# Kernel optimization log

Hardware: AMD Instinct MI355X
Metric: run time of the kernel (lower is better)

## Reference

```python
import jax, jax.numpy as jnp
import numpy as np

NUM_CLASSES = 1000
B, Q, N = 64, 900, 30
NO_OBJ_W = 0.1
COST_CLASS, COST_BBOX, COST_GIOU = 1.0, 5.0, 2.0
LOSS_BBOX, LOSS_GIOU = 5.0, 2.0


def cxcywh_to_xyxy(b):
    cx, cy, w, h = b[..., 0], b[..., 1], b[..., 2], b[..., 3]
    return jnp.stack([cx - 0.5 * w, cy - 0.5 * h, cx + 0.5 * w, cy + 0.5 * h], axis=-1)


def _area(b):
    return jnp.clip(b[..., 2] - b[..., 0], 0.0) * jnp.clip(b[..., 3] - b[..., 1], 0.0)


def giou_xyxy(b1, b2):
    # GIoU over broadcastable [..., 4] xyxy boxes
    lt = jnp.maximum(b1[..., :2], b2[..., :2])
    rb = jnp.minimum(b1[..., 2:], b2[..., 2:])
    wh = jnp.clip(rb - lt, 0.0)
    inter = wh[..., 0] * wh[..., 1]
    union = _area(b1) + _area(b2) - inter
    iou = inter / jnp.maximum(union, 1e-6)
    ltc = jnp.minimum(b1[..., :2], b2[..., :2])
    rbc = jnp.maximum(b1[..., 2:], b2[..., 2:])
    whc = jnp.clip(rbc - ltc, 0.0)
    ac = whc[..., 0] * whc[..., 1]
    return iou - (ac - union) / jnp.maximum(ac, 1e-6)


def _cost_matrices(pred_logits, pred_boxes, tgt_labels, tgt_boxes_xyxy):
    prob = jax.nn.softmax(pred_logits, axis=-1)                    # [B,Q,C+1]
    cost_cls = -jax.vmap(lambda p, l: p[:, l])(prob, tgt_labels)   # [B,Q,N]
    pred_xyxy = jnp.clip(cxcywh_to_xyxy(pred_boxes), 0.0, 1.0)     # [B,Q,4]
    cost_l1 = jnp.sum(jnp.abs(pred_xyxy[:, :, None] - tgt_boxes_xyxy[:, None]), -1)
    cost_g = -giou_xyxy(pred_xyxy[:, :, None], tgt_boxes_xyxy[:, None])
    C = COST_CLASS * cost_cls + COST_BBOX * cost_l1 + COST_GIOU * cost_g
    return C, pred_xyxy


def greedy_match(C):
    # faithful to the module's torch fallback matcher: iteratively pick the
    # global minimum of the cost matrix, masking used rows/cols (host-side,
    # non-differentiable, exactly like the detach->cpu->assignment in torch)
    Cw = C.copy()
    Qn, Nn = Cw.shape
    rows, cols = [], []
    for _ in range(min(Qn, Nn)):
        i = int(np.argmin(Cw))
        pi, ti = divmod(i, Nn)
        rows.append(pi)
        cols.append(ti)
        Cw[pi, :] = 1e9
        Cw[:, ti] = 1e9
    return np.array(rows, dtype=np.int32), np.array(cols, dtype=np.int32)


def match_all(Cnp):
    pis, tis = zip(*[greedy_match(Cnp[b]) for b in range(Cnp.shape[0])])
    return jnp.asarray(np.stack(pis)), jnp.asarray(np.stack(tis))  # [B,N] each


def set_losses(pred_logits, pred_xyxy, tgt_labels, tgt_boxes_xyxy, pi, ti):
    ce_weight = jnp.ones(NUM_CLASSES + 1, jnp.float32).at[NUM_CLASSES].set(NO_OBJ_W)
    bidx = jnp.arange(B)[:, None]
    # target class per query: matched -> tgt label, else no-object class
    tc = jnp.full((B, Q), NUM_CLASSES, dtype=jnp.int32)
    tc = tc.at[bidx, pi].set(jnp.take_along_axis(tgt_labels, ti, axis=1))
    nll = -jnp.take_along_axis(jax.nn.log_softmax(pred_logits, -1), tc[..., None].astype(jnp.int32), axis=2)[..., 0]
    w = ce_weight[tc]
    ce = jnp.mean(jnp.sum(w * nll, axis=1) / jnp.sum(w, axis=1))  # torch weighted CE mean, per image
    p_m = pred_xyxy[bidx, pi]          # [B,N,4] matched preds
    t_m = tgt_boxes_xyxy[bidx, ti]     # [B,N,4] matched targets
    l1 = jnp.mean(jnp.mean(jnp.abs(p_m - t_m), axis=(1, 2)))
    gl = jnp.mean(jnp.mean(1.0 - giou_xyxy(p_m, t_m), axis=1))
    total = ce + LOSS_BBOX * l1 + LOSS_GIOU * gl
    return jnp.stack([total, ce, l1, gl])


def setup_inputs():
    key = jax.random.key(0)
    k1, k2, k3, k4, k5 = jax.random.split(key, 5)
    pred_logits = jax.random.normal(k1, (B, Q, NUM_CLASSES + 1), jnp.float32)
    pred_boxes = jax.random.uniform(k2, (B, Q, 4), jnp.float32, 0.05, 0.95)
    tgt_labels = jax.random.randint(k3, (B, N), 0, NUM_CLASSES, dtype=jnp.int32)
    lt = jax.random.uniform(k4, (B, N, 2), jnp.float32, 0.0, 0.6)
    wh = jax.random.uniform(k5, (B, N, 2), jnp.float32, 0.02, 0.37)
    tgt_boxes_xyxy = jnp.concatenate([lt, lt + wh], axis=-1)  # valid 0..1 xyxy
    return {"pred_logits": pred_logits, "pred_boxes": pred_boxes,
            "tgt_labels": tgt_labels, "tgt_boxes_xyxy": tgt_boxes_xyxy}


def reference(pred_logits, pred_boxes, tgt_labels, tgt_boxes_xyxy):
    C, pred_xyxy = _cost_matrices(pred_logits, pred_boxes, tgt_labels, tgt_boxes_xyxy)
    pi, ti = match_all(np.asarray(jax.lax.stop_gradient(C)))
    # returns [loss_total, loss_ce, loss_bbox, loss_giou]
    return set_losses(pred_logits, pred_xyxy, tgt_labels, tgt_boxes_xyxy, pi, ti)
```

## Files before the change

kernel.cpp:

```cpp
#include <hip/hip_runtime.h>
#include <math.h>

#define BB 64
#define QQ 900
#define NN 30
#define C1 1001
#define QN (QQ * NN)
#define NO_OBJ_W 0.1f

__device__ unsigned g_ord[BB * QN];
__device__ unsigned long long g_top[BB * NN * NN];
__device__ float  g_logZ[BB * QQ];
__device__ float  g_noobj[BB * QQ];
__device__ float4 g_xyxy[BB * QQ];
__device__ float  g_acc[3];
__device__ unsigned g_cnt;

__device__ __forceinline__ float giou_f(float ax1, float ay1, float ax2, float ay2,
                                        float bx1, float by1, float bx2, float by2) {
    float ix1 = fmaxf(ax1, bx1), iy1 = fmaxf(ay1, by1);
    float ix2 = fminf(ax2, bx2), iy2 = fminf(ay2, by2);
    float iw = fmaxf(ix2 - ix1, 0.f), ih = fmaxf(iy2 - iy1, 0.f);
    float inter = iw * ih;
    float areaA = fmaxf(ax2 - ax1, 0.f) * fmaxf(ay2 - ay1, 0.f);
    float areaB = fmaxf(bx2 - bx1, 0.f) * fmaxf(by2 - by1, 0.f);
    float uni = areaA + areaB - inter;
    float iou = inter / fmaxf(uni, 1e-6f);
    float cx1 = fminf(ax1, bx1), cy1 = fminf(ay1, by1);
    float cx2 = fmaxf(ax2, bx2), cy2 = fmaxf(ay2, by2);
    float cw = fmaxf(cx2 - cx1, 0.f), ch = fmaxf(cy2 - cy1, 0.f);
    float ac = cw * ch;
    return iou - (ac - uni) / fmaxf(ac, 1e-6f);
}

__device__ __forceinline__ unsigned ord_map(float f) {
    unsigned u = __float_as_uint(f);
    return (u & 0x80000000u) ? ~u : (u | 0x80000000u);
}

__global__ __launch_bounds__(256) void cost_kernel(const float* __restrict__ logits,
                                                   const float* __restrict__ pboxes,
                                                   const int*   __restrict__ labels,
                                                   const float* __restrict__ tboxes) {
    if (blockIdx.x == 0 && threadIdx.x == 0) {
        g_acc[0] = 0.f; g_acc[1] = 0.f; g_acc[2] = 0.f;
        g_cnt = 0u;
    }
    int gwave = (blockIdx.x * blockDim.x + threadIdx.x) >> 6;
    int lane = threadIdx.x & 63;
    if (gwave >= BB * QQ) return;
    int b = gwave / QQ;

    size_t s = (size_t)gwave * C1;
    size_t a0 = (s + 3) >> 2;
    size_t a1 = (s + C1) >> 2;
    int nq = (int)(a1 - a0);
    int hh = (int)(a0 * 4 - s);
    int tt = (int)((s + C1) - a1 * 4);
    const float4* L4 = (const float4*)logits;

    float4 v4[4];
#pragma unroll
    for (int i = 0; i < 4; ++i) {
        int qq = lane + 64 * i;
        v4[i] = (qq < nq) ? L4[a0 + qq]
                          : make_float4(-INFINITY, -INFINITY, -INFINITY, -INFINITY);
    }
    float e1 = (lane < hh) ? logits[s + lane] : -INFINITY;
    float e2 = (lane < tt) ? logits[a1 * 4 + lane] : -INFINITY;

    float mx = fmaxf(e1, e2);
#pragma unroll
    for (int i = 0; i < 4; ++i)
        mx = fmaxf(mx, fmaxf(fmaxf(v4[i].x, v4[i].y), fmaxf(v4[i].z, v4[i].w)));
#pragma unroll
    for (int off = 32; off; off >>= 1) mx = fmaxf(mx, __shfl_xor(mx, off));

    float sm = __expf(e1 - mx) + __expf(e2 - mx);
#pragma unroll
    for (int i = 0; i < 4; ++i) {
        sm += __expf(v4[i].x - mx);
        sm += __expf(v4[i].y - mx);
        sm += __expf(v4[i].z - mx);
        sm += __expf(v4[i].w - mx);
    }
#pragma unroll
    for (int off = 32; off; off >>= 1) sm += __shfl_xor(sm, off);
    float logZ = mx + __logf(sm);

    float row1000 = logits[s + 1000];

    const float* pb = pboxes + (size_t)gwave * 4;
    float cx = pb[0], cy = pb[1], w = pb[2], h = pb[3];
    float x1 = fminf(fmaxf(cx - 0.5f * w, 0.f), 1.f);
    float y1 = fminf(fmaxf(cy - 0.5f * h, 0.f), 1.f);
    float x2 = fminf(fmaxf(cx + 0.5f * w, 0.f), 1.f);
    float y2 = fminf(fmaxf(cy + 0.5f * h, 0.f), 1.f);

    if (lane == 0) {
        g_logZ[gwave] = logZ;
        g_noobj[gwave] = logZ - row1000;
        g_xyxy[gwave] = make_float4(x1, y1, x2, y2);
    }

    if (lane < NN) {
        int t = lane;
        int lab = labels[b * NN + t];
        float pcls = __expf(logits[s + lab] - logZ);
        const float* tb = tboxes + ((size_t)(b * NN + t)) * 4;
        float tx1 = tb[0], ty1 = tb[1], tx2 = tb[2], ty2 = tb[3];
        float l1 = fabsf(x1 - tx1) + fabsf(y1 - ty1) + fabsf(x2 - tx2) + fabsf(y2 - ty2);
        float g = giou_f(x1, y1, x2, y2, tx1, ty1, tx2, ty2);
        g_ord[(size_t)gwave * NN + t] = ord_map(-pcls + 5.0f * l1 - 2.0f * g);
    }
}

__global__ __launch_bounds__(256) void select_kernel() {
    int gw = (blockIdx.x * blockDim.x + threadIdx.x) >> 6;
    int lane = threadIdx.x & 63;
    if (gw >= BB * NN) return;
    int b = gw / NN;
    int t = gw - b * NN;

    unsigned long long key[16];
    if (lane < 60) {
#pragma unroll
        for (int j = 0; j < 15; ++j) {
            int q = j * 60 + lane;
            unsigned o = g_ord[((size_t)(b * QQ + q)) * NN + t];
            key[j] = ((unsigned long long)o << 32) | (unsigned)(q * NN + t);
        }
    } else {
#pragma unroll
        for (int j = 0; j < 15; ++j) key[j] = ~0ull;
    }
    key[15] = ~0ull;

#pragma unroll
    for (int kk = 2; kk <= 16; kk <<= 1) {
#pragma unroll
        for (int jj = kk >> 1; jj > 0; jj >>= 1) {
#pragma unroll
            for (int i = 0; i < 16; ++i) {
                int l = i ^ jj;
                if (l > i) {
                    bool up = ((i & kk) == 0);
                    unsigned long long a = key[i], c = key[l];
                    bool sw = up ? (a > c) : (a < c);
                    key[i] = sw ? c : a;
                    key[l] = sw ? a : c;
                }
            }
        }
    }

    unsigned long long* outp = g_top + (size_t)gw * NN;
#pragma unroll 1
    for (int r = 0; r < NN / 2; ++r) {
        unsigned long long m1 = key[0];
        unsigned long long m2 = key[1];
#pragma unroll
        for (int off = 32; off; off >>= 1) {
            unsigned long long o1 = __shfl_xor(m1, off);
            unsigned long long o2 = __shfl_xor(m2, off);
            unsigned long long lo = (o1 < m1) ? o1 : m1;
            unsigned long long hi = (o1 < m1) ? m1 : o1;
            unsigned long long n2 = (o2 < m2) ? o2 : m2;
            m1 = lo;
            m2 = (hi < n2) ? hi : n2;
        }
        if (lane == 2 * r)     outp[2 * r]     = m1;
        if (lane == 2 * r + 1) outp[2 * r + 1] = m2;
        if (key[0] == m1 || key[0] == m2) {
#pragma unroll
            for (int j = 0; j < 15; ++j) key[j] = key[j + 1];
            key[15] = ~0ull;
        }
        if (key[0] == m2) {
#pragma unroll
            for (int j = 0; j < 15; ++j) key[j] = key[j + 1];
            key[15] = ~0ull;
        }
    }
}

__global__ __launch_bounds__(256) void match_loss_kernel(const float* __restrict__ logits,
                                                         const int*   __restrict__ labels,
                                                         const float* __restrict__ tboxes,
                                                         float* __restrict__ out) {
    int b = blockIdx.x;
    int tid = threadIdx.x;

    __shared__ unsigned long long s_cand[NN * NN];
    __shared__ int s_pi[NN], s_ti[NN];
    __shared__ unsigned s_dead[29];
    __shared__ float s4[4][4];

    const unsigned long long* topb = g_top + (size_t)b * NN * NN;
    for (int i = tid; i < NN * NN; i += 256) s_cand[i] = topb[i];
    if (tid < 29) s_dead[tid] = 0u;
    __syncthreads();

    if (tid < 64) {
        int lane = tid;
        bool colLive = lane < NN;
        int ptr = 0;
        unsigned long long cand = colLive ? s_cand[lane * NN] : ~0ull;
        unsigned rowc = colLive ? ((unsigned)cand) / NN : 0u;

        int it = 0;
        while (it < NN) {
            unsigned long long m1 = colLive ? cand : ~0ull;
            unsigned long long m2 = ~0ull;
#pragma unroll
            for (int off = 32; off; off >>= 1) {
                unsigned long long o1 = __shfl_xor(m1, off);
                unsigned long long o2 = __shfl_xor(m2, off);
                unsigned long long lo = (o1 < m1) ? o1 : m1;
                unsigned long long hi = (o1 < m1) ? m1 : o1;
                unsigned long long n2 = (o2 < m2) ? o2 : m2;
                m1 = lo;
                m2 = (hi < n2) ? hi : n2;
            }
            unsigned e1 = (unsigned)m1;
            int q1 = e1 / NN, t1 = e1 - (e1 / NN) * NN;
            unsigned e2 = (unsigned)m2;
            int q2 = e2 / NN, t2 = e2 - (e2 / NN) * NN;
            bool acc2 = (m2 != ~0ull) && (it + 1 < NN) && (q2 != q1) && (t2 != t1);

            if (lane == 0) {
                s_pi[it] = q1;
                s_ti[it] = t1;
                s_dead[q1 >> 5] |= (1u << (q1 & 31));
                if (acc2) {
                    s_pi[it + 1] = q2;
                    s_ti[it + 1] = t2;
                    s_dead[q2 >> 5] |= (1u << (q2 & 31));
                }
            }
            if (lane == t1) colLive = false;
            if (acc2 && lane == t2) colLive = false;
            if (colLive && (rowc == (unsigned)q1 || (acc2 && rowc == (unsigned)q2))) {
                do {
                    ++ptr;
                    cand = s_cand[lane * NN + ptr];
                    rowc = ((unsigned)cand) / NN;
                } while ((s_dead[rowc >> 5] >> (rowc & 31)) & 1u);
            }
            it += acc2 ? 2 : 1;
        }
    }
    __syncthreads();

    float sA = 0.f;
    for (int q = tid; q < QQ; q += 256) sA += g_noobj[b * QQ + q];

    float sB = 0.f, sL = 0.f, sG = 0.f;
    if (tid < NN) {
        int pq = s_pi[tid], pt = s_ti[tid];
        int gq = b * QQ + pq;
        int lab = labels[b * NN + pt];
        float mnll = g_logZ[gq] - logits[(size_t)gq * C1 + lab];
        sB = mnll - NO_OBJ_W * g_noobj[gq];
        float4 p = g_xyxy[gq];
        const float* tb = tboxes + ((size_t)(b * NN + pt)) * 4;
        float tx1 = tb[0], ty1 = tb[1], tx2 = tb[2], ty2 = tb[3];
        sL = fabsf(p.x - tx1) + fabsf(p.y - ty1) + fabsf(p.z - tx2) + fabsf(p.w - ty2);
        sG = 1.0f - giou_f(p.x, p.y, p.z, p.w, tx1, ty1, tx2, ty2);
    }

    int lane = tid & 63, wid = tid >> 6;
    float vv[4] = {sA, sB, sL, sG};
#pragma unroll
    for (int j = 0; j < 4; ++j) {
        float x = vv[j];
#pragma unroll
        for (int off = 32; off; off >>= 1) x += __shfl_xor(x, off);
        if (lane == 0) s4[wid][j] = x;
    }
    __syncthreads();
    if (tid == 0) {
        float a = 0.f, bs = 0.f, l = 0.f, g = 0.f;
        for (int w = 0; w < 4; ++w) { a += s4[w][0]; bs += s4[w][1]; l += s4[w][2]; g += s4[w][3]; }
        atomicAdd(&g_acc[0], NO_OBJ_W * a + bs);
        atomicAdd(&g_acc[1], l);
        atomicAdd(&g_acc[2], g);
        __threadfence();
        unsigned prev = atomicAdd(&g_cnt, 1u);
        if (prev == BB - 1) {
            __threadfence();
            float ce = atomicAdd(&g_acc[0], 0.f) / (float)(BB * 117);
            float l1 = atomicAdd(&g_acc[1], 0.f) / (float)(BB * NN * 4);
            float gl = atomicAdd(&g_acc[2], 0.f) / (float)(BB * NN);
            out[0] = ce + 5.0f * l1 + 2.0f * gl;
            out[1] = ce;
            out[2] = l1;
            out[3] = gl;
        }
    }
}

extern "C" void kernel_launch(void* const* d_in, const int* in_sizes, int n_in,
                              void* d_out, int out_size, void* d_ws, size_t ws_size,
                              hipStream_t stream) {
    const float* pred_logits = (const float*)d_in[0];
    const float* pred_boxes  = (const float*)d_in[1];
    const int*   tgt_labels  = (const int*)d_in[2];
    const float* tgt_boxes   = (const float*)d_in[3];
    float* out = (float*)d_out;

    cost_kernel<<<(BB * QQ) / 4, 256, 0, stream>>>(pred_logits, pred_boxes, tgt_labels, tgt_boxes);
    select_kernel<<<(BB * NN) / 4, 256, 0, stream>>>();
    match_loss_kernel<<<BB, 256, 0, stream>>>(pred_logits, tgt_labels, tgt_boxes, out);
}
```

Measured before the change: 94.44 us.

## Fuse top-k selection into matching kernel with LDS-staged cost ordering

```diff
diff --git a/kernel.cpp b/kernel.cpp
--- a/kernel.cpp
+++ b/kernel.cpp
@@ -7,9 +7,10 @@
 #define C1 1001
 #define QN (QQ * NN)
 #define NO_OBJ_W 0.1f
+#define MTB 512
+#define LDW 31
 
 __device__ unsigned g_ord[BB * QN];
-__device__ unsigned long long g_top[BB * NN * NN];
 __device__ float  g_logZ[BB * QQ];
 __device__ float  g_noobj[BB * QQ];
 __device__ float4 g_xyxy[BB * QQ];
@@ -115,94 +116,100 @@
     }
 }
 
-__global__ __launch_bounds__(256) void select_kernel() {
-    int gw = (blockIdx.x * blockDim.x + threadIdx.x) >> 6;
-    int lane = threadIdx.x & 63;
-    if (gw >= BB * NN) return;
-    int b = gw / NN;
-    int t = gw - b * NN;
-
-    unsigned long long key[16];
-    if (lane < 60) {
-#pragma unroll
-        for (int j = 0; j < 15; ++j) {
-            int q = j * 60 + lane;
-            unsigned o = g_ord[((size_t)(b * QQ + q)) * NN + t];
-            key[j] = ((unsigned long long)o << 32) | (unsigned)(q * NN + t);
-        }
-    } else {
-#pragma unroll
-        for (int j = 0; j < 15; ++j) key[j] = ~0ull;
-    }
-    key[15] = ~0ull;
-
-#pragma unroll
-    for (int kk = 2; kk <= 16; kk <<= 1) {
-#pragma unroll
-        for (int jj = kk >> 1; jj > 0; jj >>= 1) {
-#pragma unroll
-            for (int i = 0; i < 16; ++i) {
-                int l = i ^ jj;
-                if (l > i) {
-                    bool up = ((i & kk) == 0);
-                    unsigned long long a = key[i], c = key[l];
-                    bool sw = up ? (a > c) : (a < c);
-                    key[i] = sw ? c : a;
-                    key[l] = sw ? a : c;
-                }
-            }
-        }
-    }
-
-    unsigned long long* outp = g_top + (size_t)gw * NN;
-#pragma unroll 1
-    for (int r = 0; r < NN / 2; ++r) {
-        unsigned long long m1 = key[0];
-        unsigned long long m2 = key[1];
-#pragma unroll
-        for (int off = 32; off; off >>= 1) {
-            unsigned long long o1 = __shfl_xor(m1, off);
-            unsigned long long o2 = __shfl_xor(m2, off);
-            unsigned long long lo = (o1 < m1) ? o1 : m1;
-            unsigned long long hi = (o1 < m1) ? m1 : o1;
-            unsigned long long n2 = (o2 < m2) ? o2 : m2;
-            m1 = lo;
-            m2 = (hi < n2) ? hi : n2;
-        }
-        if (lane == 2 * r)     outp[2 * r]     = m1;
-        if (lane == 2 * r + 1) outp[2 * r + 1] = m2;
-        if (key[0] == m1 || key[0] == m2) {
-#pragma unroll
-            for (int j = 0; j < 15; ++j) key[j] = key[j + 1];
-            key[15] = ~0ull;
-        }
-        if (key[0] == m2) {
-#pragma unroll
-            for (int j = 0; j < 15; ++j) key[j] = key[j + 1];
-            key[15] = ~0ull;
-        }
-    }
-}
-
-__global__ __launch_bounds__(256) void match_loss_kernel(const float* __restrict__ logits,
-                                                         const int*   __restrict__ labels,
-                                                         const float* __restrict__ tboxes,
-                                                         float* __restrict__ out) {
+__global__ __launch_bounds__(MTB, 1) void sml_kernel(const float* __restrict__ logits,
+                                                     const int*   __restrict__ labels,
+                                                     const float* __restrict__ tboxes,
+                                                     float* __restrict__ out) {
     int b = blockIdx.x;
     int tid = threadIdx.x;
-
+    int lane = tid & 63, wid = tid >> 6;
+
+    __shared__ unsigned s_ord[QQ * LDW];
     __shared__ unsigned long long s_cand[NN * NN];
     __shared__ int s_pi[NN], s_ti[NN];
     __shared__ unsigned s_dead[29];
-    __shared__ float s4[4][4];
-
-    const unsigned long long* topb = g_top + (size_t)b * NN * NN;
-    for (int i = tid; i < NN * NN; i += 256) s_cand[i] = topb[i];
+    __shared__ float s4[MTB / 64][4];
+
+    const uint4* src4 = (const uint4*)(g_ord + (size_t)b * QN);
+    for (int i = tid; i < QN / 4; i += MTB) {
+        uint4 v = src4[i];
+        int f = 4 * i;
+        int q = f / NN, t = f - q * NN;
+        unsigned vals[4] = {v.x, v.y, v.z, v.w};
+#pragma unroll
+        for (int k = 0; k < 4; ++k) {
+            int fk = f + k;
+            int qk = fk / NN, tk = fk - qk * NN;
+            s_ord[qk * LDW + tk] = vals[k];
+        }
+    }
+    __syncthreads();
+
+    for (int c = wid; c < NN; c += MTB / 64) {
+        unsigned long long key[16];
+        if (lane < 60) {
+#pragma unroll
+            for (int j = 0; j < 15; ++j) {
+                int q = j * 60 + lane;
+                unsigned o = s_ord[q * LDW + c];
+                key[j] = ((unsigned long long)o << 32) | (unsigned)(q * NN + c);
+            }
+        } else {
+#pragma unroll
+            for (int j = 0; j < 15; ++j) key[j] = ~0ull;
+        }
+        key[15] = ~0ull;
+
+#pragma unroll
+        for (int kk = 2; kk <= 16; kk <<= 1) {
+#pragma unroll
+            for (int jj = kk >> 1; jj > 0; jj >>= 1) {
+#pragma unroll
+                for (int i = 0; i < 16; ++i) {
+                    int l = i ^ jj;
+                    if (l > i) {
+                        bool up = ((i & kk) == 0);
+                        unsigned long long a = key[i], cc = key[l];
+                        bool sw = up ? (a > cc) : (a < cc);
+                        key[i] = sw ? cc : a;
+                        key[l] = sw ? a : cc;
+                    }
+                }
+            }
+        }
+
+#pragma unroll 1
+        for (int r = 0; r < NN / 2; ++r) {
+            unsigned long long m1 = key[0];
+            unsigned long long m2 = key[1];
+#pragma unroll
+            for (int off = 32; off; off >>= 1) {
+                unsigned long long o1 = __shfl_xor(m1, off);
+                unsigned long long o2 = __shfl_xor(m2, off);
+                unsigned long long lo = (o1 < m1) ? o1 : m1;
+                unsigned long long hi = (o1 < m1) ? m1 : o1;
+                unsigned long long n2 = (o2 < m2) ? o2 : m2;
+                m1 = lo;
+                m2 = (hi < n2) ? hi : n2;
+            }
+            if (lane == 2 * r)     s_cand[c * NN + 2 * r]     = m1;
+            if (lane == 2 * r + 1) s_cand[c * NN + 2 * r + 1] = m2;
+            if (key[0] == m1 || key[0] == m2) {
+#pragma unroll
+                for (int j = 0; j < 15; ++j) key[j] = key[j + 1];
+                key[15] = ~0ull;
+            }
+            if (key[0] == m2) {
+#pragma unroll
+                for (int j = 0; j < 15; ++j) key[j] = key[j + 1];
+                key[15] = ~0ull;
+            }
+        }
+    }
     if (tid < 29) s_dead[tid] = 0u;
     __syncthreads();
 
     if (tid < 64) {
-        int lane = tid;
         bool colLive = lane < NN;
         int ptr = 0;
         unsigned long long cand = colLive ? s_cand[lane * NN] : ~0ull;
@@ -253,7 +260,7 @@
     __syncthreads();
 
     float sA = 0.f;
-    for (int q = tid; q < QQ; q += 256) sA += g_noobj[b * QQ + q];
+    for (int q = tid; q < QQ; q += MTB) sA += g_noobj[b * QQ + q];
 
     float sB = 0.f, sL = 0.f, sG = 0.f;
     if (tid < NN) {
@@ -269,7 +276,6 @@
         sG = 1.0f - giou_f(p.x, p.y, p.z, p.w, tx1, ty1, tx2, ty2);
     }
 
-    int lane = tid & 63, wid = tid >> 6;
     float vv[4] = {sA, sB, sL, sG};
 #pragma unroll
     for (int j = 0; j < 4; ++j) {
@@ -281,7 +287,9 @@
     __syncthreads();
     if (tid == 0) {
         float a = 0.f, bs = 0.f, l = 0.f, g = 0.f;
-        for (int w = 0; w < 4; ++w) { a += s4[w][0]; bs += s4[w][1]; l += s4[w][2]; g += s4[w][3]; }
+        for (int w = 0; w < MTB / 64; ++w) {
+            a += s4[w][0]; bs += s4[w][1]; l += s4[w][2]; g += s4[w][3];
+        }
         atomicAdd(&g_acc[0], NO_OBJ_W * a + bs);
         atomicAdd(&g_acc[1], l);
         atomicAdd(&g_acc[2], g);
@@ -310,6 +318,5 @@
     float* out = (float*)d_out;
 
     cost_kernel<<<(BB * QQ) / 4, 256, 0, stream>>>(pred_logits, pred_boxes, tgt_labels, tgt_boxes);
-    select_kernel<<<(BB * NN) / 4, 256, 0, stream>>>();
-    match_loss_kernel<<<BB, 256, 0, stream>>>(pred_logits, tgt_labels, tgt_boxes, out);
-}
+    sml_kernel<<<BB, MTB, 0, stream>>>(pred_logits, tgt_labels, tgt_boxes, out);
+}
```

New measurement: 124.0 us. 31.3% more time.
